# Kernel tuning notes

Measured on AMD Instinct MI355X. Metric: run time of the kernel, lower is better.

## Reference

```python
import jax, jax.numpy as jnp
import numpy as np

# Coefficient form of the 16 differentiable binary logic ops:
# op(a,b) = c0 + c1*a + c2*b + c3*a*b  (algebraically identical to bin_op_s's stacked einsum)
_COEF_NP = np.array([
    [0, 0, 0, 0],    # 0: zeros
    [0, 0, 0, 1],    # 1: a*b
    [0, 1, 0, -1],   # 2: a*(1-b)
    [0, 1, 0, 0],    # 3: a
    [0, 0, 1, -1],   # 4: (1-a)*b
    [0, 0, 1, 0],    # 5: b
    [0, 1, 1, -2],   # 6: xor
    [0, 1, 1, -1],   # 7: or
    [1, -1, -1, 1],  # 8: nor
    [1, -1, -1, 2],  # 9: xnor
    [1, 0, -1, 0],   # 10: 1-b
    [1, 0, -1, 1],   # 11: b=>a
    [1, -1, 0, 0],   # 12: 1-a
    [1, -1, 0, 1],   # 13: a=>b
    [1, 0, 0, -1],   # 14: nand
    [1, 0, 0, 0],    # 15: ones
], dtype=np.float32)
COEF = jnp.asarray(_COEF_NP)

TREE_DEPTH = 3
NUM_CLASSES = 10
TAU = 10.0
K = 32
BATCH = 128


def _conv_tree(x, leaf_idx, w):
    # x: [B,C,H,W]; leaf_idx: [O,8] int32 into C*9 unfolded patch dim; w: [O,7,16]
    B, C, H, W = x.shape
    xp = jnp.pad(x, ((0, 0), (0, 0), (1, 1), (1, 1)))
    # unfold (kernel=3, stride=1, pad=1): torch ordering is c*9 + spatial
    pats = jnp.stack([xp[:, :, di:di + H, dj:dj + W]
                      for di in range(3) for dj in range(3)], axis=2)  # [B,C,9,H,W]
    pats = pats.reshape(B, C * 9, H * W).transpose(0, 2, 1)            # [B,L,C*9]
    cur = pats[:, :, leaf_idx]                                         # [B,L,O,8]
    sw = jax.nn.softmax(w, axis=-1)                                    # training-mode soft gates
    coef = jnp.einsum('ogk,kc->ogc', sw, COEF)                         # [O,7,4]
    for level in range(TREE_DEPTH):
        a = cur[..., 0::2]
        b = cur[..., 1::2]                                             # [B,L,O,n]
        n = a.shape[-1]
        off = 2 ** level - 1                                           # faithful to original gate indexing
        c = coef[:, off:off + n]                                       # [O,n,4]
        cur = c[..., 0] + c[..., 1] * a + c[..., 2] * b + c[..., 3] * (a * b)
    out = cur[..., 0]                                                  # [B,L,O]
    return out.transpose(0, 2, 1).reshape(B, -1, H, W)


def _orpool(x):
    B, C, H, W = x.shape
    return x.reshape(B, C, H // 2, 2, W // 2, 2).max(axis=(3, 5))


def _difflogic(x, ca, cb, w):
    # x: [B,D]; ca/cb: [O]; w: [O,16]
    a = x[:, ca]
    b = x[:, cb]
    c = jax.nn.softmax(w, axis=-1) @ COEF                              # [O,4]
    return c[:, 0] + c[:, 1] * a + c[:, 2] * b + c[:, 3] * (a * b)


def _forward(x, w1, w2, w3, w4, fw1, fw2, fw3,
             l1, l2, l3, l4, ca1, cb1, ca2, cb2, ca3, cb3):
    # threshold-encode to 9 binary channels (bilinear resize to 32x32 is identity here)
    xb = jnp.concatenate([(x > (i + 1) / 4).astype(jnp.float32) for i in range(3)], axis=1)
    h = xb
    for li, w in ((l1, w1), (l2, w2), (l3, w3), (l4, w4)):
        h = _orpool(_conv_tree(h, li, w))
    h = h.reshape(h.shape[0], -1)                                      # [B, 4096]
    h = _difflogic(h, ca1, cb1, fw1)
    h = _difflogic(h, ca2, cb2, fw2)
    h = _difflogic(h, ca3, cb3, fw3)
    return h.reshape(h.shape[0], NUM_CLASSES, -1).sum(-1) / TAU


def _make_leaf_idx(in_ch, out_ch, rng):
    idx = np.zeros((out_ch, 8), np.int32)
    for c in range(out_ch):
        chans = rng.permutation(in_ch)[:2]
        parts = [ch * 9 + rng.permutation(9)[:4] for ch in chans]
        idx[c] = np.concatenate(parts)
    return jnp.asarray(idx)


def _unique_connections(in_dim, out_dim, rng):
    x = np.arange(in_dim, dtype=np.int64)
    a, b = x[::2], x[1::2]
    m = min(len(a), len(b)); a, b = a[:m], b[:m]
    if len(a) < out_dim:
        a = np.concatenate([a, x[1::2]]); b = np.concatenate([b, x[2::2]])
        m = min(len(a), len(b)); a, b = a[:m], b[:m]
    offset = 2
    while out_dim > len(a) > offset:
        a = np.concatenate([a, x[:-offset]]); b = np.concatenate([b, x[offset:]])
        offset += 1
    a, b = a[:out_dim], b[:out_dim]
    perm = rng.permutation(out_dim)
    return jnp.asarray(a[perm]), jnp.asarray(b[perm])


def setup_inputs() -> dict:
    key = jax.random.key(0)
    rng = np.random.default_rng(0)
    ks = jax.random.split(key, 8)
    x = jax.random.uniform(ks[0], (BATCH, 3, 32, 32), dtype=jnp.float32)
    chans = [(9, K), (K, 4 * K), (4 * K, 16 * K), (16 * K, 32 * K)]
    w1, w2, w3, w4 = [jax.random.normal(ks[1 + i], (oc, 7, 16), dtype=jnp.float32)
                      for i, (_, oc) in enumerate(chans)]
    l1, l2, l3, l4 = [_make_leaf_idx(ic, oc, rng) for ic, oc in chans]
    fc_in = 32 * K * 4
    fdims = [(fc_in, 1280 * K), (1280 * K, 640 * K), (640 * K, 320 * K)]
    fw1, fw2, fw3 = [jax.random.normal(ks[5 + i], (od, 16), dtype=jnp.float32)
                     for i, (_, od) in enumerate(fdims)]
    (ca1, cb1), (ca2, cb2), (ca3, cb3) = [_unique_connections(i, o, rng) for i, o in fdims]
    return dict(x=x, w1=w1, w2=w2, w3=w3, w4=w4, fw1=fw1, fw2=fw2, fw3=fw3,
                l1=l1, l2=l2, l3=l3, l4=l4,
                ca1=ca1, cb1=cb1, ca2=ca2, cb2=cb2, ca3=ca3, cb3=cb3)


def reference(x, w1, w2, w3, w4, fw1, fw2, fw3,
              l1, l2, l3, l4, ca1, cb1, ca2, cb2, ca3, cb3):
    return _forward(x, w1, w2, w3, w4, fw1, fw2, fw3,
                    l1, l2, l3, l4, ca1, cb1, ca2, cb2, ca3, cb3)
```

## Files before the change

kernel.cpp:

```cpp
#include <hip/hip_runtime.h>
#include <math.h>


typedef _Float16 h16;
typedef _Float16 h2 __attribute__((ext_vector_type(2)));

__constant__ float c_coef_tbl[16][4] = {
    {0, 0, 0, 0}, {0, 0, 0, 1}, {0, 1, 0, -1}, {0, 1, 0, 0},
    {0, 0, 1, -1}, {0, 0, 1, 0}, {0, 1, 1, -2}, {0, 1, 1, -1},
    {1, -1, -1, 1}, {1, -1, -1, 2}, {1, 0, -1, 0}, {1, 0, -1, 1},
    {1, -1, 0, 0}, {1, -1, 0, 1}, {1, 0, 0, -1}, {1, 0, 0, 0}};

__device__ __forceinline__ float4 softmax_coef(const float* __restrict__ wr) {
  float m = -1e30f;
#pragma unroll
  for (int k = 0; k < 16; ++k) m = fmaxf(m, wr[k]);
  float e[16], s = 0.f;
#pragma unroll
  for (int k = 0; k < 16; ++k) { e[k] = __expf(wr[k] - m); s += e[k]; }
  float inv = 1.f / s;
  float c0 = 0.f, c1 = 0.f, c2 = 0.f, c3 = 0.f;
#pragma unroll
  for (int k = 0; k < 16; ++k) {
    c0 += e[k] * c_coef_tbl[k][0];
    c1 += e[k] * c_coef_tbl[k][1];
    c2 += e[k] * c_coef_tbl[k][2];
    c3 += e[k] * c_coef_tbl[k][3];
  }
  return make_float4(c0 * inv, c1 * inv, c2 * inv, c3 * inv);
}

__device__ __forceinline__ float gate_eval(float4 c, float a, float b) {
  return c.x + c.y * a + c.z * b + c.w * (a * b);
}
__device__ __forceinline__ float4 dec_cf(uint2 u) {
  h2 p0, p1;
  *(unsigned*)&p0 = u.x;
  *(unsigned*)&p1 = u.y;
  return make_float4((float)p0[0], (float)p0[1], (float)p1[0], (float)p1[1]);
}
__device__ __forceinline__ h2 gateh(const h2* c, h2 a, h2 b) {
  return c[0] + c[1] * a + c[2] * b + c[3] * (a * b);
}

__global__ void prep_all(const float* __restrict__ w1, const float* __restrict__ w2,
                         const float* __restrict__ w3, const float* __restrict__ w4,
                         const float* __restrict__ fw1, const float* __restrict__ fw2,
                         const float* __restrict__ fw3,
                         const int* __restrict__ ca1, const int* __restrict__ cb1,
                         const int* __restrict__ ca2, const int* __restrict__ cb2,
                         const int* __restrict__ ca3, const int* __restrict__ cb3,
                         float4* __restrict__ coefC,
                         unsigned short* __restrict__ midx16,
                         _Float16* __restrict__ mcoefh) {
  int g = blockIdx.x * blockDim.x + threadIdx.x;
  if (g < 71680) {
    int o = g / 7;
    int s = g - o * 7;
    float4 c;
    if (s < 4) {
      int k = (s < 2) ? ca3[o] : cb3[o];
      int j = (s & 1) ? cb2[k] : ca2[k];
      midx16[o * 8 + s * 2]     = (unsigned short)ca1[j];
      midx16[o * 8 + s * 2 + 1] = (unsigned short)cb1[j];
      c = softmax_coef(fw1 + j * 16);
    } else if (s < 6) {
      int k = (s == 4) ? ca3[o] : cb3[o];
      c = softmax_coef(fw2 + k * 16);
    } else {
      c = softmax_coef(fw3 + o * 16);
    }
    _Float16* mc = mcoefh + o * 28 + s * 4;
    mc[0] = (_Float16)c.x; mc[1] = (_Float16)c.y;
    mc[2] = (_Float16)c.z; mc[3] = (_Float16)c.w;
  } else if (g < 78464) {
    int gg = g - 71680;
    int base = gg;
    const float* w;
    if (gg < 128)       {             w = w1; }
    else if (gg < 640)  { gg -= 128;  w = w2; }
    else if (gg < 2688) { gg -= 640;  w = w3; }
    else                { gg -= 2688; w = w4; }
    coefC[base] = softmax_coef(w + ((gg >> 2) * 7 + (gg & 3)) * 16);
  }
}

template <int C, int H, int W, int OC, int IPS, int OPS, bool OUTDUP>
__device__ void stage(const h2* __restrict__ in, h2* __restrict__ outD,
                      h16* __restrict__ outP,
                      const int* __restrict__ leaf,
                      const float4* __restrict__ coef, int tid) {
  constexpr int Wp = W + 2;
  constexpr int PH = H / 2, PW = W / 2;
  constexpr int NPOS = PH * PW;
  constexpr int TPO = 1024 / OC;
  constexpr int ITER = NPOS / TPO;
  constexpr int OWp = PW + 2;

  int oc = tid / TPO;
  int lane = tid % TPO;

  int toff[8];
#pragma unroll
  for (int l = 0; l < 8; ++l) {
    int k = leaf[oc * 8 + l];
    int cc = k / 9;
    int p = k - 9 * cc;
    int di = p / 3;
    int dj = p - 3 * di;
    toff[l] = cc * IPS + di * Wp + dj;
  }
  h2 ch[4][4];
#pragma unroll
  for (int r = 0; r < 4; ++r) {
    float4 c = coef[oc * 4 + r];
    _Float16 x0 = (_Float16)c.x, x1 = (_Float16)c.y,
             x2 = (_Float16)c.z, x3 = (_Float16)c.w;
    ch[r][0][0] = x0; ch[r][0][1] = x0;
    ch[r][1][0] = x1; ch[r][1][1] = x1;
    ch[r][2][0] = x2; ch[r][2][1] = x2;
    ch[r][3][0] = x3; ch[r][3][1] = x3;
  }

#pragma unroll
  for (int it = 0; it < ITER; ++it) {
    int pos = lane + it * TPO;
    int pw = pos % PW, ph = pos / PW;
    h2 o01[2];
#pragma unroll
    for (int py = 0; py < 2; ++py) {
      int pbase = (2 * ph + py) * Wp + 2 * pw;
      h2 lv[8];
#pragma unroll
      for (int l = 0; l < 8; ++l) lv[l] = in[toff[l] + pbase];
      h2 t0 = gateh(ch[0], lv[0], lv[1]);
      h2 t1 = gateh(ch[1], lv[2], lv[3]);
      h2 t2 = gateh(ch[2], lv[4], lv[5]);
      h2 t3 = gateh(ch[3], lv[6], lv[7]);
      h2 u0 = gateh(ch[1], t0, t1);
      h2 u1 = gateh(ch[2], t2, t3);
      o01[py] = gateh(ch[3], u0, u1);
    }
    _Float16 m0 = o01[0][0] > o01[1][0] ? o01[0][0] : o01[1][0];
    _Float16 m1 = o01[0][1] > o01[1][1] ? o01[0][1] : o01[1][1];
    _Float16 v = m0 > m1 ? m0 : m1;
    if (OUTDUP) {
      h16* oh = (h16*)outD;
      int cell = oc * OPS + (ph + 1) * OWp + (pw + 1);
      oh[2 * cell] = v;
      oh[2 * cell - 1] = v;
    } else {
      outP[oc * NPOS + ph * PW + pw] = v;
    }
  }
}

__global__ __launch_bounds__(1024) void mega(
    const float* __restrict__ x, const float4* __restrict__ coefC,
    const int* __restrict__ l1, const int* __restrict__ l2,
    const int* __restrict__ l3, const int* __restrict__ l4,
    const unsigned short* __restrict__ midx16,
    const _Float16* __restrict__ mcoefh, float* __restrict__ out) {
  __shared__ __align__(16) h2 XB[9 * 1157];
  __shared__ __align__(16) h2 S1[32 * 325];
  __shared__ __align__(16) h2 S2[128 * 101];
  __shared__ __align__(16) h16 S3[512 * 16];
  __shared__ __align__(16) h16 S4[1024 * 4];
  __shared__ float red[16][5];
  int tid = threadIdx.x;
  int b = blockIdx.x >> 1;
  int role = blockIdx.x & 1;

  {
    float4* z1 = (float4*)S1;
    float4* z2 = (float4*)S2;
    float4 zz = make_float4(0.f, 0.f, 0.f, 0.f);
    for (int i = tid; i < 2600; i += 1024) z1[i] = zz;
    for (int i = tid; i < 3232; i += 1024) z2[i] = zz;
  }
  const float* xg = x + b * 3072;
  for (int cell = tid; cell < 9 * 1157; cell += 1024) {
    int c9 = cell / 1157;
    int rem = cell - c9 * 1157;
    if (rem >= 1156) continue;
    int i = rem / 34, j = rem - 34 * (rem / 34);
    int th = c9 / 3, c = c9 - 3 * th;
    float thr = (float)(th + 1) * 0.25f;
    _Float16 lo = (_Float16)0, hi = (_Float16)0;
    if (i >= 1 && i <= 32) {
      const float* row = xg + c * 1024 + (i - 1) * 32;
      if (j >= 1 && j <= 32) lo = (_Float16)((row[j - 1] > thr) ? 1.f : 0.f);
      if (j <= 31)           hi = (_Float16)((row[j] > thr) ? 1.f : 0.f);
    }
    XB[cell] = h2{lo, hi};
  }
  __syncthreads();

  stage<9, 32, 32, 32, 1157, 325, true>(XB, S1, nullptr, l1, coefC, tid);
  __syncthreads();
  stage<32, 16, 16, 128, 325, 101, true>(S1, S2, nullptr, l2, coefC + 128, tid);
  __syncthreads();
  stage<128, 8, 8, 512, 101, 0, false>(S2, nullptr, S3, l3, coefC + 640, tid);
  __syncthreads();

  {
    int oc = tid;
    int cc[8], di[8], dj[8];
#pragma unroll
    for (int l = 0; l < 8; ++l) {
      int k = l4[oc * 8 + l];
      cc[l] = k / 9;
      int p = k - 9 * cc[l];
      di[l] = p / 3;
      dj[l] = p - 3 * di[l];
    }
    float4 c0 = coefC[2688 + oc * 4 + 0];
    float4 c1 = coefC[2688 + oc * 4 + 1];
    float4 c2 = coefC[2688 + oc * 4 + 2];
    float4 c3 = coefC[2688 + oc * 4 + 3];
#pragma unroll
    for (int pos = 0; pos < 4; ++pos) {
      int pw = pos & 1, ph = pos >> 1;
      float best = -1e30f;
#pragma unroll
      for (int py = 0; py < 2; ++py) {
#pragma unroll
        for (int px = 0; px < 2; ++px) {
          int i = 2 * ph + py, j = 2 * pw + px;
          float lv[8];
#pragma unroll
          for (int l = 0; l < 8; ++l) {
            int ii = i + di[l] - 1, jj = j + dj[l] - 1;
            float v = 0.f;
            if ((unsigned)ii < 4u && (unsigned)jj < 4u)
              v = (float)S3[cc[l] * 16 + ii * 4 + jj];
            lv[l] = v;
          }
          float t0 = gate_eval(c0, lv[0], lv[1]);
          float t1 = gate_eval(c1, lv[2], lv[3]);
          float t2 = gate_eval(c2, lv[4], lv[5]);
          float t3 = gate_eval(c3, lv[6], lv[7]);
          float u0 = gate_eval(c1, t0, t1);
          float u1 = gate_eval(c2, t2, t3);
          best = fmaxf(best, gate_eval(c3, u0, u1));
        }
      }
      S4[oc * 4 + pos] = (h16)best;
    }
  }
  __syncthreads();

  const uint4* mi = (const uint4*)midx16;
  const uint2* mc = (const uint2*)mcoefh;
  int wid = tid >> 6;
#pragma unroll
  for (int k = 0; k < 5; ++k) {
    int o = (role * 5 + k) * 1024 + tid;
    uint4 I = mi[o];
    const uint2* cfp = mc + o * 7;
    float L0 = gate_eval(dec_cf(cfp[0]), (float)S4[I.x & 0xffff], (float)S4[I.x >> 16]);
    float L1 = gate_eval(dec_cf(cfp[1]), (float)S4[I.y & 0xffff], (float)S4[I.y >> 16]);
    float L2 = gate_eval(dec_cf(cfp[2]), (float)S4[I.z & 0xffff], (float)S4[I.z >> 16]);
    float L3 = gate_eval(dec_cf(cfp[3]), (float)S4[I.w & 0xffff], (float)S4[I.w >> 16]);
    float M0 = gate_eval(dec_cf(cfp[4]), L0, L1);
    float M1 = gate_eval(dec_cf(cfp[5]), L2, L3);
    float y = gate_eval(dec_cf(cfp[6]), M0, M1);
#pragma unroll
    for (int m = 32; m > 0; m >>= 1) y += __shfl_xor(y, m, 64);
    if ((tid & 63) == 0) red[wid][k] = y;
  }
  __syncthreads();
  if (tid < 5) {
    float s = 0.f;
#pragma unroll
    for (int w = 0; w < 16; ++w) s += red[w][tid];
    out[b * 10 + role * 5 + tid] = s * 0.1f;
  }
}

extern "C" void kernel_launch(void* const* d_in, const int* in_sizes, int n_in,
                              void* d_out, int out_size, void* d_ws, size_t ws_size,
                              hipStream_t stream) {
  const float* x   = (const float*)d_in[0];
  const float* w1  = (const float*)d_in[1];
  const float* w2  = (const float*)d_in[2];
  const float* w3  = (const float*)d_in[3];
  const float* w4  = (const float*)d_in[4];
  const float* fw1 = (const float*)d_in[5];
  const float* fw2 = (const float*)d_in[6];
  const float* fw3 = (const float*)d_in[7];
  const int* l1  = (const int*)d_in[8];
  const int* l2  = (const int*)d_in[9];
  const int* l3  = (const int*)d_in[10];
  const int* l4  = (const int*)d_in[11];
  const int* ca1 = (const int*)d_in[12];
  const int* cb1 = (const int*)d_in[13];
  const int* ca2 = (const int*)d_in[14];
  const int* cb2 = (const int*)d_in[15];
  const int* ca3 = (const int*)d_in[16];
  const int* cb3 = (const int*)d_in[17];

  char* ws = (char*)d_ws;
  float4*         coefC  = (float4*)ws;
  unsigned short* midx16 = (unsigned short*)(ws + 108544);
  _Float16*       mcoefh = (_Float16*)(ws + 108544 + 163840);

  prep_all<<<307, 256, 0, stream>>>(w1, w2, w3, w4, fw1, fw2, fw3,
                                    ca1, cb1, ca2, cb2, ca3, cb3,
                                    coefC, midx16, mcoefh);
  mega<<<256, 1024, 0, stream>>>(x, coefC, l1, l2, l3, l4, midx16, mcoefh,
                                 (float*)d_out);
}
```

Measured before the change: 59.50 us.

## Store stage-3 output in padded duplicated layout and vectorize stage-4 in fp16

Stage 3 now writes its pooled output into a padded, pair-duplicated h2 layout that reuses the XB buffer, instead of a separate compact S3 array. Stage 4 can then load h2 pairs with only a row bounds check and evaluate the gate tree with packed fp16 math, rather than scalar fp32 gathers with 2D bounds checks. The stage loop is also restructured to issue both pooling rows' loads together. This cuts shared memory use and stage-4 instruction count. The cost is lower precision in stage 4 and the extra zeroing of the padding inside XB.

```diff
diff --git a/kernel.cpp b/kernel.cpp
--- a/kernel.cpp
+++ b/kernel.cpp
@@ -41,6 +41,34 @@
 }
 __device__ __forceinline__ h2 gateh(const h2* c, h2 a, h2 b) {
   return c[0] + c[1] * a + c[2] * b + c[3] * (a * b);
+}
+__device__ __forceinline__ h2 tree8(const h2 (&ch)[4][4], const h2* lv) {
+  h2 t0 = gateh(ch[0], lv[0], lv[1]);
+  h2 t1 = gateh(ch[1], lv[2], lv[3]);
+  h2 t2 = gateh(ch[2], lv[4], lv[5]);
+  h2 t3 = gateh(ch[3], lv[6], lv[7]);
+  h2 u0 = gateh(ch[1], t0, t1);
+  h2 u1 = gateh(ch[2], t2, t3);
+  return gateh(ch[3], u0, u1);
+}
+__device__ __forceinline__ h2 pkmax(h2 a, h2 b) {
+  h2 r;
+  r[0] = a[0] > b[0] ? a[0] : b[0];
+  r[1] = a[1] > b[1] ? a[1] : b[1];
+  return r;
+}
+__device__ __forceinline__ void splat_ch(const float4* __restrict__ coef, int oc,
+                                         h2 (&ch)[4][4]) {
+#pragma unroll
+  for (int r = 0; r < 4; ++r) {
+    float4 c = coef[oc * 4 + r];
+    _Float16 x0 = (_Float16)c.x, x1 = (_Float16)c.y,
+             x2 = (_Float16)c.z, x3 = (_Float16)c.w;
+    ch[r][0][0] = x0; ch[r][0][1] = x0;
+    ch[r][1][0] = x1; ch[r][1][1] = x1;
+    ch[r][2][0] = x2; ch[r][2][1] = x2;
+    ch[r][3][0] = x3; ch[r][3][1] = x3;
+  }
 }
 
 __global__ void prep_all(const float* __restrict__ w1, const float* __restrict__ w2,
@@ -85,9 +113,8 @@
   }
 }
 
-template <int C, int H, int W, int OC, int IPS, int OPS, bool OUTDUP>
+template <int C, int H, int W, int OC, int IPS, int OPS, int OW, int VH>
 __device__ void stage(const h2* __restrict__ in, h2* __restrict__ outD,
-                      h16* __restrict__ outP,
                       const int* __restrict__ leaf,
                       const float4* __restrict__ coef, int tid) {
   constexpr int Wp = W + 2;
@@ -95,7 +122,6 @@
   constexpr int NPOS = PH * PW;
   constexpr int TPO = 1024 / OC;
   constexpr int ITER = NPOS / TPO;
-  constexpr int OWp = PW + 2;
 
   int oc = tid / TPO;
   int lane = tid % TPO;
@@ -111,47 +137,28 @@
     toff[l] = cc * IPS + di * Wp + dj;
   }
   h2 ch[4][4];
-#pragma unroll
-  for (int r = 0; r < 4; ++r) {
-    float4 c = coef[oc * 4 + r];
-    _Float16 x0 = (_Float16)c.x, x1 = (_Float16)c.y,
-             x2 = (_Float16)c.z, x3 = (_Float16)c.w;
-    ch[r][0][0] = x0; ch[r][0][1] = x0;
-    ch[r][1][0] = x1; ch[r][1][1] = x1;
-    ch[r][2][0] = x2; ch[r][2][1] = x2;
-    ch[r][3][0] = x3; ch[r][3][1] = x3;
-  }
+  splat_ch(coef, oc, ch);
 
 #pragma unroll
   for (int it = 0; it < ITER; ++it) {
     int pos = lane + it * TPO;
     int pw = pos % PW, ph = pos / PW;
-    h2 o01[2];
-#pragma unroll
-    for (int py = 0; py < 2; ++py) {
-      int pbase = (2 * ph + py) * Wp + 2 * pw;
-      h2 lv[8];
-#pragma unroll
-      for (int l = 0; l < 8; ++l) lv[l] = in[toff[l] + pbase];
-      h2 t0 = gateh(ch[0], lv[0], lv[1]);
-      h2 t1 = gateh(ch[1], lv[2], lv[3]);
-      h2 t2 = gateh(ch[2], lv[4], lv[5]);
-      h2 t3 = gateh(ch[3], lv[6], lv[7]);
-      h2 u0 = gateh(ch[1], t0, t1);
-      h2 u1 = gateh(ch[2], t2, t3);
-      o01[py] = gateh(ch[3], u0, u1);
-    }
-    _Float16 m0 = o01[0][0] > o01[1][0] ? o01[0][0] : o01[1][0];
-    _Float16 m1 = o01[0][1] > o01[1][1] ? o01[0][1] : o01[1][1];
-    _Float16 v = m0 > m1 ? m0 : m1;
-    if (OUTDUP) {
-      h16* oh = (h16*)outD;
-      int cell = oc * OPS + (ph + 1) * OWp + (pw + 1);
-      oh[2 * cell] = v;
-      oh[2 * cell - 1] = v;
-    } else {
-      outP[oc * NPOS + ph * PW + pw] = v;
-    }
+    int pb0 = (2 * ph) * Wp + 2 * pw;
+    h2 A[8], B[8];
+#pragma unroll
+    for (int l = 0; l < 8; ++l) {
+      const h2* p = in + toff[l] + pb0;
+      A[l] = p[0];
+      B[l] = p[Wp];
+    }
+    h2 oA = tree8(ch, A);
+    h2 oB = tree8(ch, B);
+    h2 pm = pkmax(oA, oB);
+    _Float16 v = pm[0] > pm[1] ? pm[0] : pm[1];
+    h16* oh = (h16*)outD;
+    int cell = oc * OPS + (ph + VH) * OW + (pw + 1);
+    oh[2 * cell] = v;
+    oh[2 * cell - 1] = v;
   }
 }
 
@@ -164,9 +171,9 @@
   __shared__ __align__(16) h2 XB[9 * 1157];
   __shared__ __align__(16) h2 S1[32 * 325];
   __shared__ __align__(16) h2 S2[128 * 101];
-  __shared__ __align__(16) h16 S3[512 * 16];
   __shared__ __align__(16) h16 S4[1024 * 4];
   __shared__ float red[16][5];
+  h2* S3d = XB;
   int tid = threadIdx.x;
   int b = blockIdx.x >> 1;
   int role = blockIdx.x & 1;
@@ -196,56 +203,50 @@
   }
   __syncthreads();
 
-  stage<9, 32, 32, 32, 1157, 325, true>(XB, S1, nullptr, l1, coefC, tid);
-  __syncthreads();
-  stage<32, 16, 16, 128, 325, 101, true>(S1, S2, nullptr, l2, coefC + 128, tid);
-  __syncthreads();
-  stage<128, 8, 8, 512, 101, 0, false>(S2, nullptr, S3, l3, coefC + 640, tid);
+  stage<9, 32, 32, 32, 1157, 325, 18, 1>(XB, S1, l1, coefC, tid);
+  __syncthreads();
+
+  for (int i = tid; i < 2048; i += 1024)
+    S3d[(i >> 2) * 20 + (i & 3) * 5] = h2{(_Float16)0, (_Float16)0};
+  stage<32, 16, 16, 128, 325, 101, 10, 1>(S1, S2, l2, coefC + 128, tid);
+  __syncthreads();
+
+  stage<128, 8, 8, 512, 101, 20, 5, 0>(S2, S3d, l3, coefC + 640, tid);
   __syncthreads();
 
   {
     int oc = tid;
-    int cc[8], di[8], dj[8];
+    int boff[8], dI[8];
 #pragma unroll
     for (int l = 0; l < 8; ++l) {
       int k = l4[oc * 8 + l];
-      cc[l] = k / 9;
-      int p = k - 9 * cc[l];
-      di[l] = p / 3;
-      dj[l] = p - 3 * di[l];
-    }
-    float4 c0 = coefC[2688 + oc * 4 + 0];
-    float4 c1 = coefC[2688 + oc * 4 + 1];
-    float4 c2 = coefC[2688 + oc * 4 + 2];
-    float4 c3 = coefC[2688 + oc * 4 + 3];
+      int cc = k / 9;
+      int p = k - 9 * cc;
+      int di = p / 3;
+      int dj = p - 3 * di;
+      dI[l] = di;
+      boff[l] = cc * 20 + dj;
+    }
+    h2 ch[4][4];
+    splat_ch(coefC + 2688, oc, ch);
 #pragma unroll
     for (int pos = 0; pos < 4; ++pos) {
       int pw = pos & 1, ph = pos >> 1;
-      float best = -1e30f;
+      h2 o01[2];
 #pragma unroll
       for (int py = 0; py < 2; ++py) {
-#pragma unroll
-        for (int px = 0; px < 2; ++px) {
-          int i = 2 * ph + py, j = 2 * pw + px;
-          float lv[8];
-#pragma unroll
-          for (int l = 0; l < 8; ++l) {
-            int ii = i + di[l] - 1, jj = j + dj[l] - 1;
-            float v = 0.f;
-            if ((unsigned)ii < 4u && (unsigned)jj < 4u)
-              v = (float)S3[cc[l] * 16 + ii * 4 + jj];
-            lv[l] = v;
-          }
-          float t0 = gate_eval(c0, lv[0], lv[1]);
-          float t1 = gate_eval(c1, lv[2], lv[3]);
-          float t2 = gate_eval(c2, lv[4], lv[5]);
-          float t3 = gate_eval(c3, lv[6], lv[7]);
-          float u0 = gate_eval(c1, t0, t1);
-          float u1 = gate_eval(c2, t2, t3);
-          best = fmaxf(best, gate_eval(c3, u0, u1));
+        h2 lv[8];
+#pragma unroll
+        for (int l = 0; l < 8; ++l) {
+          int i = 2 * ph + py + dI[l] - 1;
+          h2 v = h2{(_Float16)0, (_Float16)0};
+          if ((unsigned)i < 4u) v = S3d[boff[l] + i * 5 + 2 * pw];
+          lv[l] = v;
         }
+        o01[py] = tree8(ch, lv);
       }
-      S4[oc * 4 + pos] = (h16)best;
+      h2 pm = pkmax(o01[0], o01[1]);
+      S4[oc * 4 + pos] = pm[0] > pm[1] ? pm[0] : pm[1];
     }
   }
   __syncthreads();
```

After: 58.95 us. Within noise of the previous version (-0.9%).
